# Optimization experiments

Hardware: AMD Instinct MI355X
Metric: run time of the kernel (lower is better)

## Reference

```python
import jax, jax.numpy as jnp
import numpy as np
import math

B, L = 4, 2048
D_MODEL, N_HEADS, D_K, D_V, D_FF, FACTOR = 512, 8, 64, 64, 2048, 5


def _layernorm(x, g, b, eps=1e-5):
    m = x.mean(-1, keepdims=True)
    v = jnp.mean((x - m) ** 2, axis=-1, keepdims=True)
    return (x - m) * jax.lax.rsqrt(v + eps) * g + b


def setup_inputs() -> dict:
    key = jax.random.key(0)
    ks = jax.random.split(key, 8)
    w = lambda k, shape: (jax.random.normal(k, shape, jnp.float32) * 0.02)
    sample_k = min(FACTOR * int(math.ceil(math.log(L))), L)  # c*ln(L_K) sampled keys per query
    return {
        "x": jax.random.normal(ks[0], (B, L, D_MODEL), jnp.float32),
        "Wq": w(ks[1], (D_MODEL, N_HEADS * D_K)),
        "Wk": w(ks[2], (D_MODEL, N_HEADS * D_K)),
        "Wv": w(ks[3], (D_MODEL, N_HEADS * D_V)),
        "Wo": w(ks[4], (N_HEADS * D_V, D_MODEL)),
        "ln1_g": jnp.ones((D_MODEL,), jnp.float32),
        "ln1_b": jnp.zeros((D_MODEL,), jnp.float32),
        "conv1_w": w(ks[5], (D_FF, D_MODEL)),
        "conv1_b": jnp.zeros((D_FF,), jnp.float32),
        "conv2_w": w(ks[6], (D_MODEL, D_FF)),
        "conv2_b": jnp.zeros((D_MODEL,), jnp.float32),
        "ln2_g": jnp.ones((D_MODEL,), jnp.float32),
        "ln2_b": jnp.zeros((D_MODEL,), jnp.float32),
        # Informer samples sample_k random keys per query position (constant indices)
        "sample_idx": jax.random.randint(ks[7], (L, sample_k), 0, L),
    }


def reference(x, Wq, Wk, Wv, Wo, ln1_g, ln1_b, conv1_w, conv1_b, conv2_w, conv2_b, ln2_g, ln2_b, sample_idx):
    Bx, Lx, D = x.shape
    H = N_HEADS
    # projections -> [B,H,L,d]
    Q = (x @ Wq).reshape(Bx, Lx, H, D_K).transpose(0, 2, 1, 3)
    K = (x @ Wk).reshape(Bx, Lx, H, D_K).transpose(0, 2, 1, 3)
    V = (x @ Wv).reshape(Bx, Lx, H, D_V).transpose(0, 2, 1, 3)

    u = min(FACTOR * int(math.ceil(math.log(Lx))), Lx)  # top-u active queries
    # sampled QK scores: [B,H,L,sample_k]
    K_samp = K[:, :, sample_idx]                              # [B,H,L,S,dk]
    qk_s = jnp.einsum('bhle,bhlse->bhls', Q, K_samp)
    # sparsity measure M = max - mean (Informer divides sum by L_K)
    M = qk_s.max(-1) - qk_s.sum(-1) / Lx                      # [B,H,L]
    _, top = jax.lax.top_k(M, u)                              # [B,H,u]

    Q_red = jnp.take_along_axis(Q, top[..., None], axis=2)    # [B,H,u,dk]
    scores = jnp.einsum('bhue,bhle->bhul', Q_red, K) / math.sqrt(D_K)
    attn = jax.nn.softmax(scores, axis=-1)                    # [B,H,u,L]

    # initial context = mean of V over keys; update only top-u query rows
    ctx = jnp.broadcast_to(V.mean(axis=2, keepdims=True), V.shape)  # [B,H,L,dv]
    upd = jnp.einsum('bhul,bhld->bhud', attn, V)              # [B,H,u,dv]
    bi = jnp.arange(Bx)[:, None, None]
    hi = jnp.arange(H)[None, :, None]
    ctx = ctx.at[bi, hi, top].set(upd)

    out = ctx.transpose(0, 2, 1, 3).reshape(Bx, Lx, H * D_V) @ Wo
    x1 = _layernorm(x + out, ln1_g, ln1_b)  # residual + norm inside attention sublayer

    # conv1d(k=1) FFN == per-token linear; dropout is identity in eval
    y = jax.nn.gelu(x1 @ conv1_w.T + conv1_b, approximate=False)
    y = y @ conv2_w.T + conv2_b
    return _layernorm(x1 + y, ln2_g, ln2_b)
```

## Files before the change

kernel.cpp:

```cpp
#include <hip/hip_runtime.h>
#include <hip/hip_bf16.h>

#define BB 4
#define LL 2048
#define DD 512
#define HH 8
#define DKK 64
#define FF 2048

typedef __bf16  bf16x8  __attribute__((ext_vector_type(8)));
typedef float   floatx4 __attribute__((ext_vector_type(4)));

__device__ __forceinline__ void async_cp16(const void* g, void* l) {
    __builtin_amdgcn_global_load_lds(
        (const __attribute__((address_space(1))) unsigned int*)g,
        (__attribute__((address_space(3))) unsigned int*)l,
        16, 0, 0);
}

__device__ __forceinline__ float gelu_f(float v) {
    float z  = v * 0.70710678118654752f;
    float az = fabsf(z);
    float t  = __builtin_amdgcn_rcpf(1.0f + 0.3275911f * az);
    float p  = ((((1.061405429f * t - 1.453152027f) * t + 1.421413741f) * t
                 - 0.284496736f) * t + 0.254829592f) * t;
    float e  = __expf(-z * z);
    float er = 1.0f - p * e;
    er = (z < 0.0f) ? -er : er;
    return 0.5f * v * (1.0f + er);
}

__global__ __launch_bounds__(256) void prep_w(
    const float* __restrict__ Wq, const float* __restrict__ Wk,
    const float* __restrict__ Wv, const float* __restrict__ Wo,
    __bf16* __restrict__ wb)
{
    const size_t SZ = (size_t)DD * DD;
    int z = blockIdx.z;
    const float* s = (z == 0) ? Wq : (z == 1) ? Wk : (z == 2) ? Wv : Wo;
    __bf16* hi; __bf16* lo = nullptr;
    if (z == 0)      { hi = wb;          lo = wb + SZ; }
    else if (z == 1) { hi = wb + 2 * SZ; lo = wb + 3 * SZ; }
    else if (z == 2) { hi = wb + 4 * SZ; }
    else             { hi = wb + 5 * SZ; }
    int idx = blockIdx.x * 256 + threadIdx.x;
    int k = idx >> 9, n = idx & 511;
    float v = s[idx];
    __bf16 h = (__bf16)v;
    hi[(size_t)n * DD + k] = h;
    if (lo) lo[(size_t)n * DD + k] = (__bf16)(v - (float)h);
}

__global__ __launch_bounds__(256) void cast_cw(
    const float* __restrict__ c1w, const float* __restrict__ c2w,
    __bf16* __restrict__ d1, __bf16* __restrict__ d2)
{
    const float* s = blockIdx.z ? c2w : c1w;
    __bf16* d = blockIdx.z ? d2 : d1;
    int idx = blockIdx.x * 256 + threadIdx.x;
    d[idx] = (__bf16)s[idx];
}

__global__ __launch_bounds__(256) void split_cast_x(
    const float* __restrict__ x, __bf16* __restrict__ xhi, __bf16* __restrict__ xlo)
{
    int idx = blockIdx.x * 256 + threadIdx.x;
    float v = x[idx];
    __bf16 h = (__bf16)v;
    xhi[idx] = h;
    xlo[idx] = (__bf16)(v - (float)h);
}

template<int ACT, bool BIAS, bool OUT_BF16>
__global__ __launch_bounds__(256) void gemm_mfma(
    const __bf16* __restrict__ A, const __bf16* __restrict__ B,
    const float* __restrict__ bias, void* __restrict__ Cv,
    int M, int N, int K)
{
    __shared__ __bf16 As[3][128 * 32];
    __shared__ __bf16 Bs[3][128 * 32];
    const int tid = threadIdx.x;
    const int wave = tid >> 6, lane = tid & 63;
    const int gx = gridDim.x;
    const int nwg = gx * gridDim.y;
    const int hw = blockIdx.y * gx + blockIdx.x;
    const int virt = ((nwg & 7) == 0) ? ((hw & 7) * (nwg >> 3) + (hw >> 3)) : hw;
    const int m0 = (virt / gx) * 128, n0 = (virt % gx) * 128;
    const int wm = (wave >> 1) * 64, wn = (wave & 1) * 64;
    const int l15 = lane & 15, kq = lane >> 4;

    auto stage = [&](int buf, int k0) {
        #pragma unroll
        for (int p = 0; p < 2; p++) {
            int c = p * 256 + tid;
            int row = c >> 2, col = (c & 3) * 8;
            async_cp16(A + (size_t)(m0 + row) * K + k0 + col, &As[buf][c * 8]);
            async_cp16(B + (size_t)(n0 + row) * K + k0 + col, &Bs[buf][c * 8]);
        }
    };

    floatx4 acc[4][4] = {};

    const int nt = K >> 5;
    stage(0, 0);
    stage(1, 32);
    int bi = 0;
    for (int t = 0; t < nt; t++) {
        int k2 = (t + 2) << 5;
        if (k2 < K) {
            int b2 = bi + 2; if (b2 >= 3) b2 -= 3;
            stage(b2, k2);
            asm volatile("s_waitcnt vmcnt(8)" ::: "memory");
        } else if (t + 1 < nt) {
            asm volatile("s_waitcnt vmcnt(4)" ::: "memory");
        } else {
            asm volatile("s_waitcnt vmcnt(0)" ::: "memory");
        }
        __builtin_amdgcn_s_barrier();
        asm volatile("" ::: "memory");
        bf16x8 af[4], bfr[4];
        #pragma unroll
        for (int i = 0; i < 4; i++)
            af[i] = *(const bf16x8*)(&As[bi][(wm + i * 16 + l15) * 32 + kq * 8]);
        #pragma unroll
        for (int j = 0; j < 4; j++)
            bfr[j] = *(const bf16x8*)(&Bs[bi][(wn + j * 16 + l15) * 32 + kq * 8]);
        #pragma unroll
        for (int i = 0; i < 4; i++)
            #pragma unroll
            for (int j = 0; j < 4; j++)
                acc[i][j] = __builtin_amdgcn_mfma_f32_16x16x32_bf16(bfr[j], af[i], acc[i][j], 0, 0, 0);
        asm volatile("" ::: "memory");
        __builtin_amdgcn_s_barrier();
        if (++bi == 3) bi = 0;
    }
    #pragma unroll
    for (int i = 0; i < 4; i++) {
        int m = m0 + wm + i * 16 + l15;
        #pragma unroll
        for (int j = 0; j < 4; j++) {
            int n = n0 + wn + j * 16 + kq * 4;
            floatx4 v4 = acc[i][j];
            if (BIAS) {
                float4 bv = *(const float4*)&bias[n];
                v4[0] += bv.x; v4[1] += bv.y; v4[2] += bv.z; v4[3] += bv.w;
            }
            if (ACT == 1) {
                v4[0] = gelu_f(v4[0]); v4[1] = gelu_f(v4[1]);
                v4[2] = gelu_f(v4[2]); v4[3] = gelu_f(v4[3]);
            }
            if (OUT_BF16) {
                union { __bf16 b[4]; uint2 u; } pk;
                pk.b[0] = (__bf16)v4[0]; pk.b[1] = (__bf16)v4[1];
                pk.b[2] = (__bf16)v4[2]; pk.b[3] = (__bf16)v4[3];
                *(uint2*)((__bf16*)Cv + (size_t)m * N + n) = pk.u;
            } else {
                *(float4*)((float*)Cv + (size_t)m * N + n) = *(float4*)&v4;
            }
        }
    }
}

__global__ __launch_bounds__(256) void gemm_mfma_split(
    const __bf16* __restrict__ Ah, const __bf16* __restrict__ Al,
    const __bf16* __restrict__ Bh, const __bf16* __restrict__ Bl,
    float* __restrict__ C, int M, int N, int K)
{
    __shared__ __bf16 Ahs[3][128 * 32];
    __shared__ __bf16 Als[3][128 * 32];
    __shared__ __bf16 Bhs[3][128 * 32];
    __shared__ __bf16 Bls[3][128 * 32];
    const int tid = threadIdx.x;
    const int wave = tid >> 6, lane = tid & 63;
    const int gx = gridDim.x;
    const int nwg = gx * gridDim.y;
    const int hw = blockIdx.y * gx + blockIdx.x;
    const int virt = ((nwg & 7) == 0) ? ((hw & 7) * (nwg >> 3) + (hw >> 3)) : hw;
    const int m0 = (virt / gx) * 128, n0 = (virt % gx) * 128;
    const int wm = (wave >> 1) * 64, wn = (wave & 1) * 64;
    const int l15 = lane & 15, kq = lane >> 4;

    auto stage = [&](int buf, int k0) {
        #pragma unroll
        for (int p = 0; p < 2; p++) {
            int c = p * 256 + tid;
            int row = c >> 2, col = (c & 3) * 8;
            size_t goA = (size_t)(m0 + row) * K + k0 + col;
            size_t goB = (size_t)(n0 + row) * K + k0 + col;
            async_cp16(Ah + goA, &Ahs[buf][c * 8]);
            async_cp16(Al + goA, &Als[buf][c * 8]);
            async_cp16(Bh + goB, &Bhs[buf][c * 8]);
            async_cp16(Bl + goB, &Bls[buf][c * 8]);
        }
    };

    floatx4 acc[4][4] = {};

    const int nt = K >> 5;
    stage(0, 0);
    stage(1, 32);
    int bi = 0;
    for (int t = 0; t < nt; t++) {
        int k2 = (t + 2) << 5;
        if (k2 < K) {
            int b2 = bi + 2; if (b2 >= 3) b2 -= 3;
            stage(b2, k2);
            asm volatile("s_waitcnt vmcnt(16)" ::: "memory");
        } else if (t + 1 < nt) {
            asm volatile("s_waitcnt vmcnt(8)" ::: "memory");
        } else {
            asm volatile("s_waitcnt vmcnt(0)" ::: "memory");
        }
        __builtin_amdgcn_s_barrier();
        asm volatile("" ::: "memory");
        bf16x8 ah[4], al[4], bh[4], bl[4];
        #pragma unroll
        for (int i = 0; i < 4; i++) {
            int off = (wm + i * 16 + l15) * 32 + kq * 8;
            ah[i] = *(const bf16x8*)(&Ahs[bi][off]);
            al[i] = *(const bf16x8*)(&Als[bi][off]);
        }
        #pragma unroll
        for (int j = 0; j < 4; j++) {
            int off = (wn + j * 16 + l15) * 32 + kq * 8;
            bh[j] = *(const bf16x8*)(&Bhs[bi][off]);
            bl[j] = *(const bf16x8*)(&Bls[bi][off]);
        }
        #pragma unroll
        for (int i = 0; i < 4; i++)
            #pragma unroll
            for (int j = 0; j < 4; j++) {
                acc[i][j] = __builtin_amdgcn_mfma_f32_16x16x32_bf16(bh[j], ah[i], acc[i][j], 0, 0, 0);
                acc[i][j] = __builtin_amdgcn_mfma_f32_16x16x32_bf16(bl[j], ah[i], acc[i][j], 0, 0, 0);
                acc[i][j] = __builtin_amdgcn_mfma_f32_16x16x32_bf16(bh[j], al[i], acc[i][j], 0, 0, 0);
            }
        asm volatile("" ::: "memory");
        __builtin_amdgcn_s_barrier();
        if (++bi == 3) bi = 0;
    }
    #pragma unroll
    for (int i = 0; i < 4; i++) {
        int m = m0 + wm + i * 16 + l15;
        #pragma unroll
        for (int j = 0; j < 4; j++) {
            int n = n0 + wn + j * 16 + kq * 4;
            *(float4*)(C + (size_t)m * N + n) = *(float4*)&acc[i][j];
        }
    }
}

__device__ __forceinline__ float dpp_sum16(float p) {
    int t;
    t = __builtin_amdgcn_update_dpp(0, __float_as_int(p), 0xB1,  0xF, 0xF, true);
    p += __int_as_float(t);
    t = __builtin_amdgcn_update_dpp(0, __float_as_int(p), 0x4E,  0xF, 0xF, true);
    p += __int_as_float(t);
    t = __builtin_amdgcn_update_dpp(0, __float_as_int(p), 0x141, 0xF, 0xF, true);
    p += __int_as_float(t);
    t = __builtin_amdgcn_update_dpp(0, __float_as_int(p), 0x140, 0xF, 0xF, true);
    p += __int_as_float(t);
    return p;
}

__global__ __launch_bounds__(256) void calc_m(
    const float* __restrict__ Q, const float* __restrict__ Kb,
    const int* __restrict__ sidx, float* __restrict__ Mo, int U)
{
    __shared__ int   js[64];
    __shared__ float red_mx[2][HH];
    __shared__ float red_sm[2][HH];
    int i = blockIdx.x;
    int b = i & 3, l = i >> 2;
    int tid = threadIdx.x;
    if (tid < U) js[tid] = sidx[l * U + tid];
    int e    = (tid & 127) * 4;
    int slot = tid >> 7;
    const float* qr = Q + ((size_t)(b * LL + l) * DD);
    float4 q = *(const float4*)(qr + e);
    const float* kbase = Kb + ((size_t)b * LL) * DD + e;
    __syncthreads();
    float mx = -1e30f, sm = 0.f;
    for (int s = slot; s < U; s += 2) {
        int j = js[s];
        float4 kv = *(const float4*)(kbase + (size_t)j * DD);
        float p = q.x * kv.x + q.y * kv.y + q.z * kv.z + q.w * kv.w;
        p = dpp_sum16(p);
        mx = fmaxf(mx, p);
        sm += p;
    }
    if ((tid & 15) == 0) {
        int head = (tid >> 4) & 7;
        red_mx[slot][head] = mx;
        red_sm[slot][head] = sm;
    }
    __syncthreads();
    if (tid < HH) {
        float m2 = fmaxf(red_mx[0][tid], red_mx[1][tid]);
        float s2 = red_sm[0][tid] + red_sm[1][tid];
        Mo[((size_t)(b * HH + tid)) * LL + l] = m2 - s2 * (1.0f / (float)LL);
    }
}

__global__ __launch_bounds__(256) void topk_k(
    const float* __restrict__ Mo, int* __restrict__ top, int U)
{
    __shared__ unsigned int hist[256];
    __shared__ unsigned int wsum[4];
    __shared__ unsigned int bc[2];
    __shared__ int ties[LL];
    __shared__ int cnt2[2];
    int bh = blockIdx.x, tid = threadIdx.x;
    int lane = tid & 63, w = tid >> 6;

    unsigned int my[8];
    #pragma unroll
    for (int i = 0; i < 8; i++) {
        unsigned int u = __float_as_uint(Mo[(size_t)bh * LL + tid + i * 256]);
        my[i] = u ^ ((u >> 31) ? 0xFFFFFFFFu : 0x80000000u);
    }

    unsigned int prefix = 0, pmask = 0;
    unsigned int need = (unsigned int)U;
    unsigned int above = 0;

    for (int pass = 0; pass < 4; pass++) {
        int shift = 24 - pass * 8;
        hist[tid] = 0;
        __syncthreads();
        #pragma unroll
        for (int i = 0; i < 8; i++) {
            unsigned int u = my[i];
            if ((u & pmask) == prefix)
                atomicAdd(&hist[(u >> shift) & 255u], 1u);
        }
        __syncthreads();
        unsigned int h = hist[tid];
        #pragma unroll
        for (int off = 1; off < 64; off <<= 1) {
            unsigned int o = __shfl_down(h, off);
            if (lane + off < 64) h += o;
        }
        if (lane == 0) wsum[w] = h;
        __syncthreads();
        unsigned int tail = 0;
        #pragma unroll
        for (int w2 = 1; w2 < 4; w2++) if (w2 > w) tail += wsum[w2];
        h += tail;
        hist[tid] = h;
        __syncthreads();
        unsigned int St = h;
        unsigned int St1 = (tid < 255) ? hist[tid + 1] : 0u;
        if (St >= need && St1 < need) { bc[0] = (unsigned int)tid; bc[1] = St1; }
        __syncthreads();
        unsigned int dig = bc[0], abv = bc[1];
        above += abv;
        need -= abv;
        prefix |= dig << shift;
        pmask |= 0xFFu << shift;
        __syncthreads();
    }

    if (tid == 0) { cnt2[0] = 0; cnt2[1] = 0; }
    __syncthreads();
    #pragma unroll
    for (int i = 0; i < 8; i++) {
        unsigned int u = my[i];
        int idx = tid + i * 256;
        if (u > prefix) {
            int pos = atomicAdd(&cnt2[0], 1);
            top[bh * U + pos] = idx;
        } else if (u == prefix) {
            int pos = atomicAdd(&cnt2[1], 1);
            ties[pos] = idx;
        }
    }
    __syncthreads();
    int tcnt = cnt2[1];
    #pragma unroll
    for (int i = 0; i < 8; i++) {
        unsigned int u = my[i];
        if (u == prefix) {
            int idx = tid + i * 256;
            int rank = 0;
            for (int j = 0; j < tcnt; j++) rank += (ties[j] < idx) ? 1 : 0;
            if (rank < (int)need) top[bh * U + (int)above + rank] = idx;
        }
    }
}

__global__ __launch_bounds__(256) void vmean_k(
    const __bf16* __restrict__ V, float* __restrict__ Vm)
{
    __shared__ float osum[4][DKK];
    int bh = blockIdx.x;
    int b = bh >> 3, h = bh & 7;
    int tid = threadIdx.x, d = tid & 63, part = tid >> 6;
    const __bf16* vp = V + ((size_t)(b * LL + part * 512) * DD + h * DKK + d);
    float s = 0.f;
    for (int i = 0; i < 512; i++) s += (float)vp[(size_t)i * DD];
    osum[part][d] = s;
    __syncthreads();
    if (tid < DKK)
        Vm[bh * DKK + tid] = (osum[0][tid] + osum[1][tid] + osum[2][tid] + osum[3][tid]) * (1.0f / (float)LL);
}

__global__ __launch_bounds__(256) void gather_qred(
    const float* __restrict__ Q, const int* __restrict__ top,
    __bf16* __restrict__ qred, int U)
{
    int bh = blockIdx.y;
    int b = bh >> 3, h = bh & 7;
    int e = blockIdx.x * 256 + threadIdx.x;
    int u = e >> 6, d = e & 63;
    float v = 0.f;
    if (u < U) {
        int l = top[bh * U + u];
        v = Q[((size_t)(b * LL + l) * DD + h * DKK) + d] * 0.125f;
    }
    qred[(size_t)bh * 48 * DKK + e] = (__bf16)v;
}

__global__ __launch_bounds__(256) void gemm_s(
    const __bf16* __restrict__ qred, const float* __restrict__ Kb,
    float* __restrict__ S)
{
    __shared__ __bf16 Qs[2 * 48 * 32];
    __shared__ __bf16 Ks[2 * 128 * 32];
    int bh = blockIdx.y, nc = blockIdx.x;
    int b = bh >> 3, h = bh & 7, l0 = nc * 128;
    int tid = threadIdx.x;
    const unsigned int* qsrc = (const unsigned int*)(qred + (size_t)bh * 48 * DKK);
    unsigned int* qdst = (unsigned int*)Qs;
    #pragma unroll
    for (int t = 0; t < 6; t++) {
        int ui = tid + t * 256;
        int u = ui >> 5, kp = ui & 31;
        int p = kp >> 4, kl2 = kp & 15;
        qdst[p * 768 + u * 16 + kl2] = qsrc[ui];
    }
    #pragma unroll
    for (int t = 0; t < 8; t++) {
        int fi = tid + t * 256;
        int row = fi >> 4, k4 = fi & 15;
        int p = k4 >> 3, kl = (k4 & 7) * 4;
        float4 kv = *(const float4*)(Kb + ((size_t)(b * LL + l0 + row) * DD + h * DKK + k4 * 4));
        __bf16* dst = Ks + p * 128 * 32 + row * 32 + kl;
        dst[0] = (__bf16)kv.x; dst[1] = (__bf16)kv.y;
        dst[2] = (__bf16)kv.z; dst[3] = (__bf16)kv.w;
    }
    __syncthreads();
    int wave = tid >> 6, lane = tid & 63, l15 = lane & 15, kq = lane >> 4;
    floatx4 acc[3][2] = {};
    #pragma unroll
    for (int p = 0; p < 2; p++) {
        bf16x8 bq[2];
        #pragma unroll
        for (int j = 0; j < 2; j++)
            bq[j] = *(const bf16x8*)(Ks + p * 4096 + (wave * 32 + j * 16 + l15) * 32 + kq * 8);
        #pragma unroll
        for (int i = 0; i < 3; i++) {
            bf16x8 aq = *(const bf16x8*)(Qs + p * 1536 + (i * 16 + l15) * 32 + kq * 8);
            #pragma unroll
            for (int j = 0; j < 2; j++)
                acc[i][j] = __builtin_amdgcn_mfma_f32_16x16x32_bf16(bq[j], aq, acc[i][j], 0, 0, 0);
        }
    }
    #pragma unroll
    for (int i = 0; i < 3; i++) {
        int row = i * 16 + l15;
        #pragma unroll
        for (int j = 0; j < 2; j++) {
            int col = l0 + wave * 32 + j * 16 + kq * 4;
            *(float4*)&S[((size_t)bh * 48 + row) * LL + col] = *(float4*)&acc[i][j];
        }
    }
}

__global__ __launch_bounds__(256) void softmax_p(float* __restrict__ S, int U)
{
    __shared__ float red[256];
    int row = blockIdx.x;
    int bh = row / U, u = row % U;
    float* sr = S + ((size_t)bh * 48 + u) * LL;
    int tid = threadIdx.x;
    float sc[8]; float mx = -1e30f;
    #pragma unroll
    for (int i = 0; i < 8; i++) { sc[i] = sr[tid + i * 256]; mx = fmaxf(mx, sc[i]); }
    red[tid] = mx; __syncthreads();
    for (int s = 128; s > 0; s >>= 1) { if (tid < s) red[tid] = fmaxf(red[tid], red[tid + s]); __syncthreads(); }
    mx = red[0]; __syncthreads();
    float se = 0.f;
    #pragma unroll
    for (int i = 0; i < 8; i++) { sc[i] = __expf(sc[i] - mx); se += sc[i]; }
    red[tid] = se; __syncthreads();
    for (int s = 128; s > 0; s >>= 1) { if (tid < s) red[tid] += red[tid + s]; __syncthreads(); }
    float inv = 1.0f / red[0];
    __bf16* pr = (__bf16*)sr;
    #pragma unroll
    for (int i = 0; i < 8; i++) pr[tid + i * 256] = (__bf16)(sc[i] * inv);
}

__global__ __launch_bounds__(256) void pv_k(
    const float* __restrict__ S, const __bf16* __restrict__ V,
    float* __restrict__ upd, int U)
{
    __shared__ __bf16 pls[4 * LL];
    __shared__ float osum[4][4][DKK];
    int bh = blockIdx.y, uc = blockIdx.x;
    int b = bh >> 3, h = bh & 7, tid = threadIdx.x;
    #pragma unroll
    for (int t = 0; t < 16; t++) {
        int ui = tid + t * 256;
        int up = ui >> 10, lw = ui & 1023;
        const unsigned int* src = (const unsigned int*)(S + ((size_t)bh * 48 + uc * 4 + up) * LL);
        ((unsigned int*)pls)[up * 1024 + lw] = src[lw];
    }
    __syncthreads();
    int d = tid & 63, part = tid >> 6;
    float a0 = 0.f, a1 = 0.f, a2 = 0.f, a3 = 0.f;
    const __bf16* vp = V + ((size_t)(b * LL + part * 512) * DD + h * DKK + d);
    int lbase = part * 512;
    for (int i = 0; i < 512; i++) {
        float v = (float)vp[(size_t)i * DD];
        int l = lbase + i;
        a0 += (float)pls[l] * v;
        a1 += (float)pls[LL + l] * v;
        a2 += (float)pls[2 * LL + l] * v;
        a3 += (float)pls[3 * LL + l] * v;
    }
    osum[part][0][d] = a0; osum[part][1][d] = a1;
    osum[part][2][d] = a2; osum[part][3][d] = a3;
    __syncthreads();
    int u2 = tid >> 6;
    float s = osum[0][u2][d] + osum[1][u2][d] + osum[2][u2][d] + osum[3][u2][d];
    upd[((size_t)bh * U + uc * 4 + u2) * DKK + d] = s;
}

__global__ __launch_bounds__(256) void ctx_init(
    const float* __restrict__ Vm, __bf16* __restrict__ ctx)
{
    int idx = blockIdx.x * 256 + threadIdx.x;
    int c = idx & 511; int h = c >> 6, d = c & 63;
    int bl = idx >> 9; int b = bl >> 11;
    ctx[idx] = (__bf16)Vm[(b * HH + h) * DKK + d];
}
__global__ __launch_bounds__(256) void ctx_scatter(
    const float* __restrict__ upd, const int* __restrict__ top,
    __bf16* __restrict__ ctx, int U, int total)
{
    int idx = blockIdx.x * 256 + threadIdx.x;
    if (idx >= total) return;
    int d = idx & 63; int ru = idx >> 6;
    int bh = ru / U, u = ru % U;
    int b = bh >> 3, h = bh & 7;
    int l = top[bh * U + u];
    ctx[(((size_t)(b * LL + l)) << 9) + h * DKK + d] = (__bf16)upd[idx];
}

__global__ __launch_bounds__(256) void ln1_k(
    const float* __restrict__ x, const float* __restrict__ aout,
    const float* __restrict__ g, const float* __restrict__ bb,
    __bf16* __restrict__ x1h)
{
    __shared__ float red[256];
    int row = blockIdx.x, tid = threadIdx.x;
    size_t base = (size_t)row * DD;
    float h0 = x[base + tid] + aout[base + tid];
    float h1 = x[base + 256 + tid] + aout[base + 256 + tid];
    red[tid] = h0 + h1; __syncthreads();
    for (int s = 128; s > 0; s >>= 1) { if (tid < s) red[tid] += red[tid + s]; __syncthreads(); }
    float mean = red[0] * (1.0f / DD); __syncthreads();
    float d0 = h0 - mean, d1 = h1 - mean;
    red[tid] = d0 * d0 + d1 * d1; __syncthreads();
    for (int s = 128; s > 0; s >>= 1) { if (tid < s) red[tid] += red[tid + s]; __syncthreads(); }
    float rstd = rsqrtf(red[0] * (1.0f / DD) + 1e-5f);
    x1h[base + tid]       = (__bf16)(d0 * rstd * g[tid] + bb[tid]);
    x1h[base + 256 + tid] = (__bf16)(d1 * rstd * g[256 + tid] + bb[256 + tid]);
}

__global__ __launch_bounds__(256) void ln2_k(
    const __bf16* __restrict__ x1h, const float* __restrict__ f2o,
    const float* __restrict__ c2b,
    const float* __restrict__ g, const float* __restrict__ bb,
    float* __restrict__ out)
{
    __shared__ float red[256];
    int row = blockIdx.x, tid = threadIdx.x;
    size_t base = (size_t)row * DD;
    float h0 = (float)x1h[base + tid] + f2o[base + tid] + c2b[tid];
    float h1 = (float)x1h[base + 256 + tid] + f2o[base + 256 + tid] + c2b[256 + tid];
    red[tid] = h0 + h1; __syncthreads();
    for (int s = 128; s > 0; s >>= 1) { if (tid < s) red[tid] += red[tid + s]; __syncthreads(); }
    float mean = red[0] * (1.0f / DD); __syncthreads();
    float d0 = h0 - mean, d1 = h1 - mean;
    red[tid] = d0 * d0 + d1 * d1; __syncthreads();
    for (int s = 128; s > 0; s >>= 1) { if (tid < s) red[tid] += red[tid + s]; __syncthreads(); }
    float rstd = rsqrtf(red[0] * (1.0f / DD) + 1e-5f);
    out[base + tid]       = d0 * rstd * g[tid] + bb[tid];
    out[base + 256 + tid] = d1 * rstd * g[256 + tid] + bb[256 + tid];
}

extern "C" void kernel_launch(void* const* d_in, const int* in_sizes, int n_in,
                              void* d_out, int out_size, void* d_ws, size_t ws_size,
                              hipStream_t stream)
{
    const float* x   = (const float*)d_in[0];
    const float* Wq  = (const float*)d_in[1];
    const float* Wk  = (const float*)d_in[2];
    const float* Wv  = (const float*)d_in[3];
    const float* Wo  = (const float*)d_in[4];
    const float* g1  = (const float*)d_in[5];
    const float* b1  = (const float*)d_in[6];
    const float* c1w = (const float*)d_in[7];
    const float* c1b = (const float*)d_in[8];
    const float* c2w = (const float*)d_in[9];
    const float* c2b = (const float*)d_in[10];
    const float* g2  = (const float*)d_in[11];
    const float* b2  = (const float*)d_in[12];
    const int* sidx  = (const int*)d_in[13];
    float* out       = (float*)d_out;

    const int U = in_sizes[13] / LL;
    const int M = BB * LL;

    char* ws = (char*)d_ws;
    const size_t MB = (size_t)1 << 20;
    float*  Q    = (float*)(ws + 0);
    float*  Kb   = (float*)(ws + 16 * MB);
    __bf16* V    = (__bf16*)(ws + 32 * MB);
    __bf16* xhi  = (__bf16*)(ws + 40 * MB);
    __bf16* xlo  = (__bf16*)(ws + 48 * MB);
    float*  S    = (float*)(ws + 40 * MB);
    __bf16* wb   = (__bf16*)(ws + 56 * MB);
    __bf16* c1wb = (__bf16*)(ws + 59 * MB);
    __bf16* c2wb = (__bf16*)(ws + 61 * MB);
    float*  Mo   = (float*)(ws + 63 * MB);
    float*  upd  = (float*)(ws + 63 * MB + 256 * 1024);
    float*  Vm   = (float*)(ws + 63 * MB + 576 * 1024);
    int*    top  = (int*)  (ws + 63 * MB + 584 * 1024);
    __bf16* qred = (__bf16*)(ws + 63 * MB + 592 * 1024);
    float*  aout = Q;
    float*  f2o  = Q;
    __bf16* ctx  = V;
    __bf16* ych  = (__bf16*)(ws + 16 * MB);
    __bf16* x1h  = xlo;
    (void)ws_size; (void)n_in; (void)out_size;

    const size_t SZ = (size_t)DD * DD;
    __bf16* WqThi = wb;          __bf16* WqTlo = wb + SZ;
    __bf16* WkThi = wb + 2 * SZ; __bf16* WkTlo = wb + 3 * SZ;
    __bf16* WvT   = wb + 4 * SZ; __bf16* WoT   = wb + 5 * SZ;

    prep_w<<<dim3(DD * DD / 256, 1, 4), 256, 0, stream>>>(Wq, Wk, Wv, Wo, wb);
    cast_cw<<<dim3(FF * DD / 256, 1, 2), 256, 0, stream>>>(c1w, c2w, c1wb, c2wb);
    split_cast_x<<<BB * LL * DD / 256, 256, 0, stream>>>(x, xhi, xlo);

    dim3 gproj(DD / 128, M / 128);
    gemm_mfma_split<<<gproj, 256, 0, stream>>>(xhi, xlo, WqThi, WqTlo, Q,  M, DD, DD);
    gemm_mfma_split<<<gproj, 256, 0, stream>>>(xhi, xlo, WkThi, WkTlo, Kb, M, DD, DD);
    gemm_mfma<0, false, true ><<<gproj, 256, 0, stream>>>(xhi, WvT, nullptr, V, M, DD, DD);

    calc_m<<<BB * LL, 256, 0, stream>>>(Q, Kb, sidx, Mo, U);
    topk_k<<<BB * HH, 256, 0, stream>>>(Mo, top, U);
    vmean_k<<<BB * HH, 256, 0, stream>>>(V, Vm);

    gather_qred<<<dim3(48 * DKK / 256, BB * HH), 256, 0, stream>>>(Q, top, qred, U);
    gemm_s<<<dim3(LL / 128, BB * HH), 256, 0, stream>>>(qred, Kb, S);
    softmax_p<<<BB * HH * U, 256, 0, stream>>>(S, U);
    pv_k<<<dim3(U / 4, BB * HH), 256, 0, stream>>>(S, V, upd, U);

    ctx_init<<<M * DD / 256, 256, 0, stream>>>(Vm, ctx);
    int sc_total = BB * HH * U * DKK;
    ctx_scatter<<<(sc_total + 255) / 256, 256, 0, stream>>>(upd, top, ctx, U, sc_total);
    gemm_mfma<0, false, false><<<gproj, 256, 0, stream>>>(ctx, WoT, nullptr, aout, M, DD, DD);

    ln1_k<<<M, 256, 0, stream>>>(x, aout, g1, b1, x1h);

    gemm_mfma<1, true,  true ><<<dim3(FF / 128, M / 128), 256, 0, stream>>>(x1h, c1wb, c1b, ych, M, FF, DD);
    gemm_mfma<0, false, false><<<dim3(DD / 128, M / 128), 256, 0, stream>>>(ych, c2wb, nullptr, f2o, M, DD, FF);

    ln2_k<<<M, 256, 0, stream>>>(x1h, f2o, c2b, g2, b2, out);
}
```

Baseline: 414.8 us.

## Replace dense output projection with per-batch base plus sparse correction; swizzle GEMM LDS

Most context rows equal the per-(b,h) mean of V, so the dense 8192x512x512 output projection is replaced by two pieces. One is a per-batch base row (mean context times Wo) broadcast to all tokens. The other is a small MFMA correction GEMM over the top-u rows, applied with atomicAdd scatter. Separately, the GEMM kernels apply an XOR swizzle to LDS tile columns to reduce bank conflicts, and move the wait/barrier to the end of each iteration so there is one barrier per k-step instead of two. Risks include atomic contention when duplicate top indices hit the same row, and bf16 rounding of the correction terms.

```diff
diff --git a/kernel.cpp b/kernel.cpp
--- a/kernel.cpp
+++ b/kernel.cpp
@@ -93,7 +93,8 @@
         #pragma unroll
         for (int p = 0; p < 2; p++) {
             int c = p * 256 + tid;
-            int row = c >> 2, col = (c & 3) * 8;
+            int row = c >> 2;
+            int col = ((c & 3) ^ ((row >> 1) & 3)) * 8;
             async_cp16(A + (size_t)(m0 + row) * K + k0 + col, &As[buf][c * 8]);
             async_cp16(B + (size_t)(n0 + row) * K + k0 + col, &Bs[buf][c * 8]);
         }
@@ -104,34 +105,36 @@
     const int nt = K >> 5;
     stage(0, 0);
     stage(1, 32);
+    asm volatile("s_waitcnt vmcnt(4)" ::: "memory");
+    __builtin_amdgcn_s_barrier();
     int bi = 0;
     for (int t = 0; t < nt; t++) {
         int k2 = (t + 2) << 5;
         if (k2 < K) {
             int b2 = bi + 2; if (b2 >= 3) b2 -= 3;
             stage(b2, k2);
-            asm volatile("s_waitcnt vmcnt(8)" ::: "memory");
-        } else if (t + 1 < nt) {
-            asm volatile("s_waitcnt vmcnt(4)" ::: "memory");
-        } else {
-            asm volatile("s_waitcnt vmcnt(0)" ::: "memory");
-        }
-        __builtin_amdgcn_s_barrier();
+        }
         asm volatile("" ::: "memory");
         bf16x8 af[4], bfr[4];
         #pragma unroll
-        for (int i = 0; i < 4; i++)
-            af[i] = *(const bf16x8*)(&As[bi][(wm + i * 16 + l15) * 32 + kq * 8]);
-        #pragma unroll
-        for (int j = 0; j < 4; j++)
-            bfr[j] = *(const bf16x8*)(&Bs[bi][(wn + j * 16 + l15) * 32 + kq * 8]);
+        for (int i = 0; i < 4; i++) {
+            int ra = wm + i * 16 + l15;
+            af[i] = *(const bf16x8*)(&As[bi][ra * 32 + ((kq ^ ((ra >> 1) & 3)) << 3)]);
+        }
+        #pragma unroll
+        for (int j = 0; j < 4; j++) {
+            int rb = wn + j * 16 + l15;
+            bfr[j] = *(const bf16x8*)(&Bs[bi][rb * 32 + ((kq ^ ((rb >> 1) & 3)) << 3)]);
+        }
         #pragma unroll
         for (int i = 0; i < 4; i++)
             #pragma unroll
             for (int j = 0; j < 4; j++)
                 acc[i][j] = __builtin_amdgcn_mfma_f32_16x16x32_bf16(bfr[j], af[i], acc[i][j], 0, 0, 0);
         asm volatile("" ::: "memory");
-        __builtin_amdgcn_s_barrier();
+        if (t + 2 < nt)      asm volatile("s_waitcnt vmcnt(4)" ::: "memory");
+        else if (t + 1 < nt) asm volatile("s_waitcnt vmcnt(0)" ::: "memory");
+        if (t + 1 < nt) __builtin_amdgcn_s_barrier();
         if (++bi == 3) bi = 0;
     }
     #pragma unroll
@@ -184,7 +187,8 @@
         #pragma unroll
         for (int p = 0; p < 2; p++) {
             int c = p * 256 + tid;
-            int row = c >> 2, col = (c & 3) * 8;
+            int row = c >> 2;
+            int col = ((c & 3) ^ ((row >> 1) & 3)) * 8;
             size_t goA = (size_t)(m0 + row) * K + k0 + col;
             size_t goB = (size_t)(n0 + row) * K + k0 + col;
             async_cp16(Ah + goA, &Ahs[buf][c * 8]);
@@ -199,30 +203,28 @@
     const int nt = K >> 5;
     stage(0, 0);
     stage(1, 32);
+    asm volatile("s_waitcnt vmcnt(8)" ::: "memory");
+    __builtin_amdgcn_s_barrier();
     int bi = 0;
     for (int t = 0; t < nt; t++) {
         int k2 = (t + 2) << 5;
         if (k2 < K) {
             int b2 = bi + 2; if (b2 >= 3) b2 -= 3;
             stage(b2, k2);
-            asm volatile("s_waitcnt vmcnt(16)" ::: "memory");
-        } else if (t + 1 < nt) {
-            asm volatile("s_waitcnt vmcnt(8)" ::: "memory");
-        } else {
-            asm volatile("s_waitcnt vmcnt(0)" ::: "memory");
-        }
-        __builtin_amdgcn_s_barrier();
+        }
         asm volatile("" ::: "memory");
         bf16x8 ah[4], al[4], bh[4], bl[4];
         #pragma unroll
         for (int i = 0; i < 4; i++) {
-            int off = (wm + i * 16 + l15) * 32 + kq * 8;
+            int ra = wm + i * 16 + l15;
+            int off = ra * 32 + ((kq ^ ((ra >> 1) & 3)) << 3);
             ah[i] = *(const bf16x8*)(&Ahs[bi][off]);
             al[i] = *(const bf16x8*)(&Als[bi][off]);
         }
         #pragma unroll
         for (int j = 0; j < 4; j++) {
-            int off = (wn + j * 16 + l15) * 32 + kq * 8;
+            int rb = wn + j * 16 + l15;
+            int off = rb * 32 + ((kq ^ ((rb >> 1) & 3)) << 3);
             bh[j] = *(const bf16x8*)(&Bhs[bi][off]);
             bl[j] = *(const bf16x8*)(&Bls[bi][off]);
         }
@@ -235,7 +237,9 @@
                 acc[i][j] = __builtin_amdgcn_mfma_f32_16x16x32_bf16(bh[j], al[i], acc[i][j], 0, 0, 0);
             }
         asm volatile("" ::: "memory");
-        __builtin_amdgcn_s_barrier();
+        if (t + 2 < nt)      asm volatile("s_waitcnt vmcnt(8)" ::: "memory");
+        else if (t + 1 < nt) asm volatile("s_waitcnt vmcnt(0)" ::: "memory");
+        if (t + 1 < nt) __builtin_amdgcn_s_barrier();
         if (++bi == 3) bi = 0;
     }
     #pragma unroll
@@ -536,25 +540,110 @@
     upd[((size_t)bh * U + uc * 4 + u2) * DKK + d] = s;
 }
 
-__global__ __launch_bounds__(256) void ctx_init(
-    const float* __restrict__ Vm, __bf16* __restrict__ ctx)
+__global__ __launch_bounds__(256) void base_k(
+    const float* __restrict__ Vm, const float* __restrict__ Wo,
+    float* __restrict__ base)
+{
+    __shared__ float cm[DD];
+    __shared__ float part[8][32];
+    int b = blockIdx.y, n0 = blockIdx.x * 32, tid = threadIdx.x;
+    cm[tid] = Vm[b * DD + tid];
+    cm[tid + 256] = Vm[b * DD + 256 + tid];
+    __syncthreads();
+    int n = n0 + (tid & 31), kg = tid >> 5;
+    float s = 0.f;
+    for (int k = kg * 64; k < kg * 64 + 64; k++) s += cm[k] * Wo[(size_t)k * DD + n];
+    part[kg][tid & 31] = s;
+    __syncthreads();
+    if (tid < 32) {
+        float t = 0.f;
+        #pragma unroll
+        for (int g = 0; g < 8; g++) t += part[g][tid];
+        base[b * DD + n0 + tid] = t;
+    }
+}
+
+__global__ __launch_bounds__(256) void aout_init(
+    const float* __restrict__ base, float* __restrict__ aout)
 {
     int idx = blockIdx.x * 256 + threadIdx.x;
-    int c = idx & 511; int h = c >> 6, d = c & 63;
-    int bl = idx >> 9; int b = bl >> 11;
-    ctx[idx] = (__bf16)Vm[(b * HH + h) * DKK + d];
-}
-__global__ __launch_bounds__(256) void ctx_scatter(
-    const float* __restrict__ upd, const int* __restrict__ top,
-    __bf16* __restrict__ ctx, int U, int total)
-{
-    int idx = blockIdx.x * 256 + threadIdx.x;
-    if (idx >= total) return;
-    int d = idx & 63; int ru = idx >> 6;
-    int bh = ru / U, u = ru % U;
-    int b = bh >> 3, h = bh & 7;
-    int l = top[bh * U + u];
-    ctx[(((size_t)(b * LL + l)) << 9) + h * DKK + d] = (__bf16)upd[idx];
+    aout[idx] = base[((idx >> 20) << 9) + (idx & 511)];
+}
+
+__global__ __launch_bounds__(256) void aw_prep(
+    const float* __restrict__ upd, const float* __restrict__ Vm,
+    __bf16* __restrict__ aw, int U)
+{
+    int bh = blockIdx.x, tid = threadIdx.x;
+    #pragma unroll
+    for (int t = 0; t < 12; t++) {
+        int e = tid + t * 256;
+        int u = e >> 6, d = e & 63;
+        float v = (u < U) ? upd[((size_t)bh * U + u) * DKK + d] - Vm[bh * DKK + d] : 0.f;
+        aw[(size_t)bh * 48 * DKK + e] = (__bf16)v;
+    }
+}
+
+__global__ __launch_bounds__(256) void corr_gemm(
+    const __bf16* __restrict__ aw, const __bf16* __restrict__ WoT,
+    const int* __restrict__ top, float* __restrict__ aout, int U)
+{
+    __shared__ __bf16 Qs[2 * 48 * 32];
+    __shared__ __bf16 Ks[2 * 128 * 32];
+    int bh = blockIdx.y, nc = blockIdx.x;
+    int b = bh >> 3, h = bh & 7, n0 = nc * 128;
+    int tid = threadIdx.x;
+    const unsigned int* qsrc = (const unsigned int*)(aw + (size_t)bh * 48 * DKK);
+    unsigned int* qdst = (unsigned int*)Qs;
+    #pragma unroll
+    for (int t = 0; t < 6; t++) {
+        int ui = tid + t * 256;
+        int u = ui >> 5, kp = ui & 31;
+        int p = kp >> 4, kl2 = kp & 15;
+        qdst[p * 768 + u * 16 + kl2] = qsrc[ui];
+    }
+    const unsigned int* wsrc = (const unsigned int*)WoT;
+    unsigned int* kdst = (unsigned int*)Ks;
+    #pragma unroll
+    for (int t = 0; t < 16; t++) {
+        int ui = tid + t * 256;
+        int row = ui >> 5, c2 = ui & 31;
+        int p = c2 >> 4, col2 = c2 & 15;
+        kdst[p * 2048 + row * 16 + col2] = wsrc[(size_t)(n0 + row) * (DD / 2) + h * 32 + c2];
+    }
+    __syncthreads();
+    int wave = tid >> 6, lane = tid & 63, l15 = lane & 15, kq = lane >> 4;
+    floatx4 acc[3][2] = {};
+    #pragma unroll
+    for (int p = 0; p < 2; p++) {
+        bf16x8 bq[2];
+        #pragma unroll
+        for (int j = 0; j < 2; j++)
+            bq[j] = *(const bf16x8*)(Ks + p * 4096 + (wave * 32 + j * 16 + l15) * 32 + kq * 8);
+        #pragma unroll
+        for (int i = 0; i < 3; i++) {
+            bf16x8 aq = *(const bf16x8*)(Qs + p * 1536 + (i * 16 + l15) * 32 + kq * 8);
+            #pragma unroll
+            for (int j = 0; j < 2; j++)
+                acc[i][j] = __builtin_amdgcn_mfma_f32_16x16x32_bf16(bq[j], aq, acc[i][j], 0, 0, 0);
+        }
+    }
+    #pragma unroll
+    for (int i = 0; i < 3; i++) {
+        int u = i * 16 + l15;
+        if (u < U) {
+            int l = top[bh * U + u];
+            float* dst = aout + ((size_t)(b * LL + l)) * DD;
+            #pragma unroll
+            for (int j = 0; j < 2; j++) {
+                int n = n0 + wave * 32 + j * 16 + kq * 4;
+                atomicAdd(dst + n,     acc[i][j][0]);
+                atomicAdd(dst + n + 1, acc[i][j][1]);
+                atomicAdd(dst + n + 2, acc[i][j][2]);
+                atomicAdd(dst + n + 3, acc[i][j][3]);
+            }
+        }
+    }
 }
 
 __global__ __launch_bounds__(256) void ln1_k(
@@ -639,9 +728,10 @@
     float*  Vm   = (float*)(ws + 63 * MB + 576 * 1024);
     int*    top  = (int*)  (ws + 63 * MB + 584 * 1024);
     __bf16* qred = (__bf16*)(ws + 63 * MB + 592 * 1024);
+    __bf16* aw   = (__bf16*)(ws + 63 * MB + 784 * 1024);
+    float*  basep= (float*)(ws + 63 * MB + 976 * 1024);
     float*  aout = Q;
     float*  f2o  = Q;
-    __bf16* ctx  = V;
     __bf16* ych  = (__bf16*)(ws + 16 * MB);
     __bf16* x1h  = xlo;
     (void)ws_size; (void)n_in; (void)out_size;
@@ -669,10 +759,10 @@
     softmax_p<<<BB * HH * U, 256, 0, stream>>>(S, U);
     pv_k<<<dim3(U / 4, BB * HH), 256, 0, stream>>>(S, V, upd, U);
 
-    ctx_init<<<M * DD / 256, 256, 0, stream>>>(Vm, ctx);
-    int sc_total = BB * HH * U * DKK;
-    ctx_scatter<<<(sc_total + 255) / 256, 256, 0, stream>>>(upd, top, ctx, U, sc_total);
-    gemm_mfma<0, false, false><<<gproj, 256, 0, stream>>>(ctx, WoT, nullptr, aout, M, DD, DD);
+    base_k<<<dim3(16, BB), 256, 0, stream>>>(Vm, Wo, basep);
+    aw_prep<<<BB * HH, 256, 0, stream>>>(upd, Vm, aw, U);
+    aout_init<<<M * DD / 256, 256, 0, stream>>>(basep, aout);
+    corr_gemm<<<dim3(DD / 128, BB * HH), 256, 0, stream>>>(aw, WoT, top, aout, U);
 
     ln1_k<<<M, 256, 0, stream>>>(x, aout, g1, b1, x1h);
 
```

Result: slower. 429.6 us (+3.6%).
